# Performance work log

Hardware: AMD Instinct MI355X
Metric: run time of the kernel (lower is better)

## Reference

```python
import jax, jax.numpy as jnp
import numpy as np

H = 8        # n_heads (== n_kv_heads)
D = 128      # head_dim
WINDOW = 16  # sliding window (left); causal => right window = 0
EPS = 1e-6   # qk_norm_eps


def rms_norm(x, w, eps=EPS):
    # RMSNorm over last dim with learnable scale
    ms = jnp.mean(jnp.square(x), axis=-1, keepdims=True)
    return x * jax.lax.rsqrt(ms + eps) * w


def setup_inputs() -> dict:
    key = jax.random.key(0)
    ks = jax.random.split(key, 5)
    B, S, dim = 4, 2048, 1024
    scale = 1.0 / np.sqrt(dim)
    return {
        "x": jax.random.normal(ks[0], (B, S, dim), jnp.float32),
        "wq": jax.random.normal(ks[1], (dim, dim), jnp.float32) * scale,
        "wk": jax.random.normal(ks[2], (dim, dim), jnp.float32) * scale,
        "wv": jax.random.normal(ks[3], (dim, dim), jnp.float32) * scale,
        "wo": jax.random.normal(ks[4], (dim, dim), jnp.float32) * scale,
        "q_norm_w": jnp.ones((dim,), jnp.float32),
        "k_norm_w": jnp.ones((dim,), jnp.float32),
    }


def reference(x, wq, wk, wv, wo, q_norm_w, k_norm_w):
    B, S, dim = x.shape
    # projections (torch Linear: x @ W.T)
    xq = rms_norm(x @ wq.T, q_norm_w)
    xk = rms_norm(x @ wk.T, k_norm_w)
    xv = x @ wv.T
    q = xq.reshape(B, S, H, D)
    k = xk.reshape(B, S, H, D)
    v = xv.reshape(B, S, H, D)

    # ALiBi slopes for 8 heads (power of two): 2^-1 .. 2^-8
    slopes = jnp.exp2(-jnp.arange(1, H + 1, dtype=jnp.float32))
    pos = jnp.arange(S)
    rel = pos[None, :] - pos[:, None]          # [S, S], rel[i, j] = j - i
    bias = slopes[:, None, None] * rel.astype(x.dtype)   # [H, S, S]
    masked = (rel > 0) | (rel < -WINDOW)       # causal + sliding window
    bias = jnp.where(masked[None], -jnp.inf, bias)

    scores = jnp.einsum('bqhd,bkhd->bhqk', q, k) / np.sqrt(D) + bias[None]
    attn = jax.nn.softmax(scores, axis=-1)
    out = jnp.einsum('bhqk,bkhd->bqhd', attn, v).reshape(B, S, H * D)
    return out @ wo.T
```

## Files before the change

### kernel.cpp

```cpp
#include <hip/hip_runtime.h>
#include <math.h>

#define NHEADS 8
#define HDIM   128
#define WIN    16
#define DIM    1024
#define QKVDIM 3072
#define SEQ    2048
#define BATCH  4
#define MROWS  (BATCH * SEQ)
#define RMS_EPS 1e-6f

typedef __bf16 bf16x8 __attribute__((ext_vector_type(8)));
typedef unsigned short u16x8 __attribute__((ext_vector_type(8)));
typedef float  f32x4  __attribute__((ext_vector_type(4)));

__device__ __forceinline__ unsigned short f2b(float f) {
    union { float f; unsigned u; } c; c.f = f;
    return (unsigned short)((c.u + 0x7FFFu + ((c.u >> 16) & 1u)) >> 16);
}
__device__ __forceinline__ float b2f(unsigned short u) {
    union { unsigned u; float f; } c; c.u = ((unsigned)u) << 16; return c.f;
}

__device__ __forceinline__ void storec(unsigned short* p, float v) { *p = f2b(v); }
__device__ __forceinline__ void storec(float* p, float v) { *p = v; }

__global__ __launch_bounds__(256) void cast_all(const float* __restrict__ x,
                                                const float* __restrict__ w0,
                                                const float* __restrict__ w1,
                                                const float* __restrict__ w2,
                                                const float* __restrict__ w3,
                                                unsigned short* __restrict__ xb,
                                                unsigned short* __restrict__ wb)
{
    const int b = blockIdx.x;
    const int t = threadIdx.x;
    const float* src;
    unsigned short* dst;
    int i;
    if (b < 8192) {
        i = b * 256 + t;
        src = x; dst = xb;
    } else {
        const int bb = b - 8192;
        const int which = bb >> 10;
        i = (bb & 1023) * 256 + t;
        src = which == 0 ? w0 : which == 1 ? w1 : which == 2 ? w2 : w3;
        dst = wb + (size_t)which * DIM * DIM;
    }
    const float4 v = ((const float4*)src)[i];
    ushort4 o;
    o.x = f2b(v.x); o.y = f2b(v.y); o.z = f2b(v.z); o.w = f2b(v.w);
    ((ushort4*)dst)[i] = o;
}

template <typename TC>
__global__ __launch_bounds__(256) void gemm_nt_mfma(const unsigned short* __restrict__ A,
                                                    const unsigned short* __restrict__ B,
                                                    TC* __restrict__ C,
                                                    int M, int N, int K)
{
    __shared__ __align__(16) __bf16 As[128 * 32];
    __shared__ __align__(16) __bf16 Bs[128 * 32];

    const int t    = threadIdx.x;
    const int w    = t >> 6;
    const int lane = t & 63;
    const int wm   = w >> 1;
    const int wn   = w & 1;
    const int bm0  = blockIdx.y * 128;
    const int bn0  = blockIdx.x * 128;

    const int sr = lane >> 2;
    const int kc = (lane & 3) * 8;

    const unsigned short* gA0 = A + (size_t)(bm0 + w * 16 + sr) * K + kc;
    const unsigned short* gA1 = gA0 + (size_t)64 * K;
    const unsigned short* gB0 = B + (size_t)(bn0 + w * 16 + sr) * K + kc;
    const unsigned short* gB1 = gB0 + (size_t)64 * K;

    __bf16* lA0 = &As[(w * 16) * 32];
    __bf16* lA1 = &As[(w * 16 + 64) * 32];
    __bf16* lB0 = &Bs[(w * 16) * 32];
    __bf16* lB1 = &Bs[(w * 16 + 64) * 32];

    const int frow = lane & 15;
    const int fk   = (lane >> 4) * 8;

    f32x4 acc[4][4];
    #pragma unroll
    for (int i = 0; i < 4; ++i)
        #pragma unroll
        for (int j = 0; j < 4; ++j)
            #pragma unroll
            for (int e = 0; e < 4; ++e) acc[i][j][e] = 0.f;

    for (int kt = 0; kt < K; kt += 32) {
        __syncthreads();
        __builtin_amdgcn_global_load_lds((const __attribute__((address_space(1))) void*)(gA0 + kt),
                                         (__attribute__((address_space(3))) void*)lA0, 16, 0, 0);
        __builtin_amdgcn_global_load_lds((const __attribute__((address_space(1))) void*)(gA1 + kt),
                                         (__attribute__((address_space(3))) void*)lA1, 16, 0, 0);
        __builtin_amdgcn_global_load_lds((const __attribute__((address_space(1))) void*)(gB0 + kt),
                                         (__attribute__((address_space(3))) void*)lB0, 16, 0, 0);
        __builtin_amdgcn_global_load_lds((const __attribute__((address_space(1))) void*)(gB1 + kt),
                                         (__attribute__((address_space(3))) void*)lB1, 16, 0, 0);
        __syncthreads();

        bf16x8 af[4], bg[4];
        #pragma unroll
        for (int i = 0; i < 4; ++i) {
            af[i] = *(const bf16x8*)&As[(wm * 64 + i * 16 + frow) * 32 + fk];
            bg[i] = *(const bf16x8*)&Bs[(wn * 64 + i * 16 + frow) * 32 + fk];
        }
        #pragma unroll
        for (int i = 0; i < 4; ++i)
            #pragma unroll
            for (int j = 0; j < 4; ++j)
                acc[i][j] = __builtin_amdgcn_mfma_f32_16x16x32_bf16(af[i], bg[j], acc[i][j], 0, 0, 0);
    }

    const int m_base = bm0 + wm * 64;
    const int n_base = bn0 + wn * 64;
    const int col    = lane & 15;
    const int rquad  = (lane >> 4) * 4;
    #pragma unroll
    for (int i = 0; i < 4; ++i)
        #pragma unroll
        for (int r = 0; r < 4; ++r) {
            TC* crow = C + (size_t)(m_base + i * 16 + rquad + r) * N + n_base + col;
            #pragma unroll
            for (int j = 0; j < 4; ++j)
                storec(crow + j * 16, acc[i][j][r]);
        }
}

__global__ __launch_bounds__(256) void rmsnorm2(unsigned short* __restrict__ xqkv,
                                                const float* __restrict__ qw,
                                                const float* __restrict__ kw)
{
    const int row   = blockIdx.x;
    const int which = blockIdx.y;
    const int t     = threadIdx.x;
    unsigned short* xr = xqkv + (size_t)row * QKVDIM + which * DIM;
    const float* w = which ? kw : qw;

    const ushort4 u = ((const ushort4*)xr)[t];
    const float4 v = make_float4(b2f(u.x), b2f(u.y), b2f(u.z), b2f(u.w));
    float ss = v.x * v.x + v.y * v.y + v.z * v.z + v.w * v.w;
    #pragma unroll
    for (int off = 32; off > 0; off >>= 1) ss += __shfl_xor(ss, off, 64);

    __shared__ float red[4];
    if ((t & 63) == 0) red[t >> 6] = ss;
    __syncthreads();
    const float total = red[0] + red[1] + red[2] + red[3];
    const float scale = rsqrtf(total * (1.0f / DIM) + RMS_EPS);

    const float4 wv = ((const float4*)w)[t];
    ushort4 o;
    o.x = f2b(v.x * scale * wv.x);
    o.y = f2b(v.y * scale * wv.y);
    o.z = f2b(v.z * scale * wv.z);
    o.w = f2b(v.w * scale * wv.w);
    ((ushort4*)xr)[t] = o;
}

__global__ __launch_bounds__(256) void attn_mfma(const unsigned short* __restrict__ qkv,
                                                 unsigned short* __restrict__ o)
{
    __shared__ __align__(16) unsigned short Klds[80 * 136];
    __shared__ __align__(16) unsigned short Vt[128 * 88];
    __shared__ __align__(16) unsigned short Plds[4 * 16 * 40];

    const int t  = threadIdx.x;
    const int qb = blockIdx.x;
    const int h  = blockIdx.y;
    const int r0 = qb * 64;
    const int i0 = r0 & (SEQ - 1);
    const int bb = r0 - i0;

    const unsigned short* kg = qkv + DIM + h * HDIM;
    const unsigned short* vg = qkv + 2 * DIM + h * HDIM;

    #pragma unroll
    for (int it = 0; it < 5; ++it) {
        const int c = it * 256 + t;
        {
            const int lr = c >> 4, c8 = c & 15;
            const int ks = i0 - 16 + lr;
            const int rc = ks < 0 ? 0 : ks;
            const u16x8 kv = *(const u16x8*)(kg + (size_t)(bb + rc) * QKVDIM + c8 * 8);
            *(u16x8*)&Klds[lr * 136 + c8 * 8] = kv;
        }
        {
            const int c8 = c / 80, lr = c - c8 * 80;
            const int ks = i0 - 16 + lr;
            const int rc = ks < 0 ? 0 : ks;
            const u16x8 vv = *(const u16x8*)(vg + (size_t)(bb + rc) * QKVDIM + c8 * 8);
            #pragma unroll
            for (int e = 0; e < 8; ++e)
                Vt[(c8 * 8 + e) * 88 + lr] = vv[e];
        }
    }
    __syncthreads();

    const int w    = t >> 6;
    const int lane = t & 63;
    const int frow = lane & 15;
    const int quad = lane >> 4;
    const int fk   = quad * 8;

    f32x4 s0 = {0.f, 0.f, 0.f, 0.f}, s1 = {0.f, 0.f, 0.f, 0.f};
    const unsigned short* qg = qkv + h * HDIM;
    const size_t qrow = (size_t)(r0 + w * 16 + frow) * QKVDIM;
    #pragma unroll
    for (int kt = 0; kt < 4; ++kt) {
        const bf16x8 af = *(const bf16x8*)(qg + qrow + kt * 32 + fk);
        const bf16x8 b0 = *(const bf16x8*)&Klds[(w * 16 + frow) * 136 + kt * 32 + fk];
        const bf16x8 b1 = *(const bf16x8*)&Klds[(w * 16 + 16 + frow) * 136 + kt * 32 + fk];
        s0 = __builtin_amdgcn_mfma_f32_16x16x32_bf16(af, b0, s0, 0, 0, 0);
        s1 = __builtin_amdgcn_mfma_f32_16x16x32_bf16(af, b1, s1, 0, 0, 0);
    }

    const float scl   = 0.088388347648318447f;
    const float slope = exp2f(-(float)(h + 1));
    const bool  lead  = (i0 == 0) && (w == 0);
    const int   col   = frow;
    float inv[4];
    #pragma unroll
    for (int r = 0; r < 4; ++r) {
        const int m = quad * 4 + r;
        float v0 = (col < m || lead) ? -1e30f : s0[r] * scl + slope * (float)(col - 16 - m);
        float v1 = (col > m)         ? -1e30f : s1[r] * scl + slope * (float)(col - m);
        float mx = fmaxf(v0, v1);
        #pragma unroll
        for (int off = 1; off < 16; off <<= 1) mx = fmaxf(mx, __shfl_xor(mx, off, 64));
        const float e0 = __expf(v0 - mx);
        const float e1 = __expf(v1 - mx);
        float sm = e0 + e1;
        #pragma unroll
        for (int off = 1; off < 16; off <<= 1) sm += __shfl_xor(sm, off, 64);
        inv[r] = 1.0f / sm;
        Plds[(w * 16 + m) * 40 + col]      = f2b(e0);
        Plds[(w * 16 + m) * 40 + 16 + col] = f2b(e1);
    }

    const bf16x8 pf = *(const bf16x8*)&Plds[(w * 16 + frow) * 40 + fk];
    f32x4 oa[8];
    #pragma unroll
    for (int nt = 0; nt < 8; ++nt) {
        oa[nt][0] = 0.f; oa[nt][1] = 0.f; oa[nt][2] = 0.f; oa[nt][3] = 0.f;
        const bf16x8 vf = *(const bf16x8*)&Vt[(nt * 16 + frow) * 88 + w * 16 + fk];
        oa[nt] = __builtin_amdgcn_mfma_f32_16x16x32_bf16(pf, vf, oa[nt], 0, 0, 0);
    }

    #pragma unroll
    for (int nt = 0; nt < 8; ++nt)
        #pragma unroll
        for (int r = 0; r < 4; ++r) {
            const int m = quad * 4 + r;
            o[(size_t)(r0 + w * 16 + m) * DIM + h * HDIM + nt * 16 + col] =
                f2b(oa[nt][r] * inv[r]);
        }
}

extern "C" void kernel_launch(void* const* d_in, const int* in_sizes, int n_in,
                              void* d_out, int out_size, void* d_ws, size_t ws_size,
                              hipStream_t stream)
{
    const float* x  = (const float*)d_in[0];
    const float* wq = (const float*)d_in[1];
    const float* wk = (const float*)d_in[2];
    const float* wv = (const float*)d_in[3];
    const float* wo = (const float*)d_in[4];
    const float* qw = (const float*)d_in[5];
    const float* kw = (const float*)d_in[6];
    float* out = (float*)d_out;

    unsigned short* xb   = (unsigned short*)d_ws;
    unsigned short* wb   = xb + (size_t)MROWS * DIM;
    unsigned short* xqkv = wb + (size_t)4 * DIM * DIM;
    unsigned short* ob   = xqkv + (size_t)MROWS * QKVDIM;
    unsigned short* wob  = wb + (size_t)3 * DIM * DIM;

    cast_all<<<12288, 256, 0, stream>>>(x, wq, wk, wv, wo, xb, wb);

    gemm_nt_mfma<unsigned short><<<dim3(QKVDIM / 128, MROWS / 128), 256, 0, stream>>>(
        xb, wb, xqkv, MROWS, QKVDIM, DIM);

    rmsnorm2<<<dim3(MROWS, 2), 256, 0, stream>>>(xqkv, qw, kw);

    attn_mfma<<<dim3(MROWS / 64, NHEADS), 256, 0, stream>>>(xqkv, ob);

    gemm_nt_mfma<float><<<dim3(DIM / 128, MROWS / 128), 256, 0, stream>>>(
        ob, wob, out, MROWS, DIM, DIM);
}
```

Baseline: 229.4 us.

## Fuse RMSNorm into GEMM epilogue and attention load; widen GEMM K tile with swizzle

The separate rmsnorm kernel is removed. The QKV GEMM epilogue now accumulates per-row sums of squares into a workspace buffer with atomics, and the attention kernel applies the normalization scale and weights to Q and K as it loads them. The cast kernel zeroes that buffer. Separately, the GEMM K tile doubles from 32 to 64, with an XOR-swizzled LDS layout to avoid bank conflicts and half as many barriers. This removes a full read-modify-write pass over Q and K, at the cost of atomics and extra math in attention. The sums of squares come from fp32 accumulators rather than rounded bf16, and K rows are renormalized redundantly across query blocks.

```diff
diff --git a/kernel.cpp b/kernel.cpp
--- a/kernel.cpp
+++ b/kernel.cpp
@@ -22,6 +22,9 @@
 __device__ __forceinline__ float b2f(unsigned short u) {
     union { unsigned u; float f; } c; c.u = ((unsigned)u) << 16; return c.f;
 }
+__device__ __forceinline__ bf16x8 u2b(u16x8 u) {
+    union { u16x8 u; bf16x8 b; } c; c.u = u; return c.b;
+}
 
 __device__ __forceinline__ void storec(unsigned short* p, float v) { *p = f2b(v); }
 __device__ __forceinline__ void storec(float* p, float v) { *p = v; }
@@ -32,10 +35,15 @@
                                                 const float* __restrict__ w2,
                                                 const float* __restrict__ w3,
                                                 unsigned short* __restrict__ xb,
-                                                unsigned short* __restrict__ wb)
+                                                unsigned short* __restrict__ wb,
+                                                float* __restrict__ sumsq)
 {
     const int b = blockIdx.x;
     const int t = threadIdx.x;
+    if (b >= 12288) {
+        ((float4*)sumsq)[(b - 12288) * 256 + t] = make_float4(0.f, 0.f, 0.f, 0.f);
+        return;
+    }
     const float* src;
     unsigned short* dst;
     int i;
@@ -59,10 +67,11 @@
 __global__ __launch_bounds__(256) void gemm_nt_mfma(const unsigned short* __restrict__ A,
                                                     const unsigned short* __restrict__ B,
                                                     TC* __restrict__ C,
+                                                    float* __restrict__ sumsq,
                                                     int M, int N, int K)
 {
-    __shared__ __align__(16) __bf16 As[128 * 32];
-    __shared__ __align__(16) __bf16 Bs[128 * 32];
+    __shared__ __align__(16) __bf16 As[128 * 64];
+    __shared__ __align__(16) __bf16 Bs[128 * 64];
 
     const int t    = threadIdx.x;
     const int w    = t >> 6;
@@ -72,21 +81,17 @@
     const int bm0  = blockIdx.y * 128;
     const int bn0  = blockIdx.x * 128;
 
-    const int sr = lane >> 2;
-    const int kc = (lane & 3) * 8;
-
-    const unsigned short* gA0 = A + (size_t)(bm0 + w * 16 + sr) * K + kc;
-    const unsigned short* gA1 = gA0 + (size_t)64 * K;
-    const unsigned short* gB0 = B + (size_t)(bn0 + w * 16 + sr) * K + kc;
-    const unsigned short* gB1 = gB0 + (size_t)64 * K;
-
-    __bf16* lA0 = &As[(w * 16) * 32];
-    __bf16* lA1 = &As[(w * 16 + 64) * 32];
-    __bf16* lB0 = &Bs[(w * 16) * 32];
-    __bf16* lB1 = &Bs[(w * 16 + 64) * 32];
+    const int lrow   = lane >> 3;
+    const int lchunk = (lane & 7) ^ (lrow & 7);
+    const size_t laneoff = (size_t)lrow * K + lchunk * 8;
+
+    const unsigned short* gA = A + (size_t)bm0 * K + laneoff;
+    const unsigned short* gB = B + (size_t)bn0 * K + laneoff;
 
     const int frow = lane & 15;
-    const int fk   = (lane >> 4) * 8;
+    const int quad = lane >> 4;
+    const int cs0 = ((quad    ) ^ (frow & 7)) * 8;
+    const int cs1 = ((quad + 4) ^ (frow & 7)) * 8;
 
     f32x4 acc[4][4];
     #pragma unroll
@@ -96,35 +101,41 @@
             #pragma unroll
             for (int e = 0; e < 4; ++e) acc[i][j][e] = 0.f;
 
-    for (int kt = 0; kt < K; kt += 32) {
+    for (int kt = 0; kt < K; kt += 64) {
         __syncthreads();
-        __builtin_amdgcn_global_load_lds((const __attribute__((address_space(1))) void*)(gA0 + kt),
-                                         (__attribute__((address_space(3))) void*)lA0, 16, 0, 0);
-        __builtin_amdgcn_global_load_lds((const __attribute__((address_space(1))) void*)(gA1 + kt),
-                                         (__attribute__((address_space(3))) void*)lA1, 16, 0, 0);
-        __builtin_amdgcn_global_load_lds((const __attribute__((address_space(1))) void*)(gB0 + kt),
-                                         (__attribute__((address_space(3))) void*)lB0, 16, 0, 0);
-        __builtin_amdgcn_global_load_lds((const __attribute__((address_space(1))) void*)(gB1 + kt),
-                                         (__attribute__((address_space(3))) void*)lB1, 16, 0, 0);
+        #pragma unroll
+        for (int s = 0; s < 4; ++s) {
+            const int seg = w * 4 + s;
+            __builtin_amdgcn_global_load_lds(
+                (const __attribute__((address_space(1))) void*)(gA + (size_t)seg * 8 * K + kt),
+                (__attribute__((address_space(3))) void*)&As[seg * 512], 16, 0, 0);
+            __builtin_amdgcn_global_load_lds(
+                (const __attribute__((address_space(1))) void*)(gB + (size_t)seg * 8 * K + kt),
+                (__attribute__((address_space(3))) void*)&Bs[seg * 512], 16, 0, 0);
+        }
         __syncthreads();
 
-        bf16x8 af[4], bg[4];
-        #pragma unroll
-        for (int i = 0; i < 4; ++i) {
-            af[i] = *(const bf16x8*)&As[(wm * 64 + i * 16 + frow) * 32 + fk];
-            bg[i] = *(const bf16x8*)&Bs[(wn * 64 + i * 16 + frow) * 32 + fk];
-        }
-        #pragma unroll
-        for (int i = 0; i < 4; ++i)
-            #pragma unroll
-            for (int j = 0; j < 4; ++j)
-                acc[i][j] = __builtin_amdgcn_mfma_f32_16x16x32_bf16(af[i], bg[j], acc[i][j], 0, 0, 0);
+        #pragma unroll
+        for (int sub = 0; sub < 2; ++sub) {
+            const int cs = sub ? cs1 : cs0;
+            bf16x8 af[4], bg[4];
+            #pragma unroll
+            for (int i = 0; i < 4; ++i) {
+                af[i] = *(const bf16x8*)&As[(wm * 64 + i * 16 + frow) * 64 + cs];
+                bg[i] = *(const bf16x8*)&Bs[(wn * 64 + i * 16 + frow) * 64 + cs];
+            }
+            #pragma unroll
+            for (int i = 0; i < 4; ++i)
+                #pragma unroll
+                for (int j = 0; j < 4; ++j)
+                    acc[i][j] = __builtin_amdgcn_mfma_f32_16x16x32_bf16(af[i], bg[j], acc[i][j], 0, 0, 0);
+        }
     }
 
     const int m_base = bm0 + wm * 64;
     const int n_base = bn0 + wn * 64;
-    const int col    = lane & 15;
-    const int rquad  = (lane >> 4) * 4;
+    const int col    = frow;
+    const int rquad  = quad * 4;
     #pragma unroll
     for (int i = 0; i < 4; ++i)
         #pragma unroll
@@ -134,40 +145,29 @@
             for (int j = 0; j < 4; ++j)
                 storec(crow + j * 16, acc[i][j][r]);
         }
-}
-
-__global__ __launch_bounds__(256) void rmsnorm2(unsigned short* __restrict__ xqkv,
-                                                const float* __restrict__ qw,
-                                                const float* __restrict__ kw)
-{
-    const int row   = blockIdx.x;
-    const int which = blockIdx.y;
-    const int t     = threadIdx.x;
-    unsigned short* xr = xqkv + (size_t)row * QKVDIM + which * DIM;
-    const float* w = which ? kw : qw;
-
-    const ushort4 u = ((const ushort4*)xr)[t];
-    const float4 v = make_float4(b2f(u.x), b2f(u.y), b2f(u.z), b2f(u.w));
-    float ss = v.x * v.x + v.y * v.y + v.z * v.z + v.w * v.w;
-    #pragma unroll
-    for (int off = 32; off > 0; off >>= 1) ss += __shfl_xor(ss, off, 64);
-
-    __shared__ float red[4];
-    if ((t & 63) == 0) red[t >> 6] = ss;
-    __syncthreads();
-    const float total = red[0] + red[1] + red[2] + red[3];
-    const float scale = rsqrtf(total * (1.0f / DIM) + RMS_EPS);
-
-    const float4 wv = ((const float4*)w)[t];
-    ushort4 o;
-    o.x = f2b(v.x * scale * wv.x);
-    o.y = f2b(v.y * scale * wv.y);
-    o.z = f2b(v.z * scale * wv.z);
-    o.w = f2b(v.w * scale * wv.w);
-    ((ushort4*)xr)[t] = o;
+
+    if (sumsq != nullptr && bn0 < 2 * DIM) {
+        const int which = bn0 >> 10;
+        #pragma unroll
+        for (int i = 0; i < 4; ++i)
+            #pragma unroll
+            for (int r = 0; r < 4; ++r) {
+                float p = acc[i][0][r] * acc[i][0][r] + acc[i][1][r] * acc[i][1][r]
+                        + acc[i][2][r] * acc[i][2][r] + acc[i][3][r] * acc[i][3][r];
+                p += __shfl_xor(p, 1, 64);
+                p += __shfl_xor(p, 2, 64);
+                p += __shfl_xor(p, 4, 64);
+                p += __shfl_xor(p, 8, 64);
+                if (frow == 0)
+                    atomicAdd(&sumsq[(size_t)(m_base + i * 16 + rquad + r) * 2 + which], p);
+            }
+    }
 }
 
 __global__ __launch_bounds__(256) void attn_mfma(const unsigned short* __restrict__ qkv,
+                                                 const float* __restrict__ sumsq,
+                                                 const float* __restrict__ qw,
+                                                 const float* __restrict__ kw,
                                                  unsigned short* __restrict__ o)
 {
     __shared__ __align__(16) unsigned short Klds[80 * 136];
@@ -191,8 +191,13 @@
             const int lr = c >> 4, c8 = c & 15;
             const int ks = i0 - 16 + lr;
             const int rc = ks < 0 ? 0 : ks;
+            const float ksc = rsqrtf(sumsq[(size_t)(bb + rc) * 2 + 1] * (1.0f / DIM) + RMS_EPS);
             const u16x8 kv = *(const u16x8*)(kg + (size_t)(bb + rc) * QKVDIM + c8 * 8);
-            *(u16x8*)&Klds[lr * 136 + c8 * 8] = kv;
+            u16x8 ko;
+            #pragma unroll
+            for (int e = 0; e < 8; ++e)
+                ko[e] = f2b(b2f(kv[e]) * ksc * kw[h * HDIM + c8 * 8 + e]);
+            *(u16x8*)&Klds[lr * 136 + c8 * 8] = ko;
         }
         {
             const int c8 = c / 80, lr = c - c8 * 80;
@@ -215,9 +220,15 @@
     f32x4 s0 = {0.f, 0.f, 0.f, 0.f}, s1 = {0.f, 0.f, 0.f, 0.f};
     const unsigned short* qg = qkv + h * HDIM;
     const size_t qrow = (size_t)(r0 + w * 16 + frow) * QKVDIM;
+    const float qsc = rsqrtf(sumsq[(size_t)(r0 + w * 16 + frow) * 2] * (1.0f / DIM) + RMS_EPS);
     #pragma unroll
     for (int kt = 0; kt < 4; ++kt) {
-        const bf16x8 af = *(const bf16x8*)(qg + qrow + kt * 32 + fk);
+        const u16x8 qa = *(const u16x8*)(qg + qrow + kt * 32 + fk);
+        u16x8 qn;
+        #pragma unroll
+        for (int e = 0; e < 8; ++e)
+            qn[e] = f2b(b2f(qa[e]) * qsc * qw[h * HDIM + kt * 32 + fk + e]);
+        const bf16x8 af = u2b(qn);
         const bf16x8 b0 = *(const bf16x8*)&Klds[(w * 16 + frow) * 136 + kt * 32 + fk];
         const bf16x8 b1 = *(const bf16x8*)&Klds[(w * 16 + 16 + frow) * 136 + kt * 32 + fk];
         s0 = __builtin_amdgcn_mfma_f32_16x16x32_bf16(af, b0, s0, 0, 0, 0);
@@ -283,17 +294,16 @@
     unsigned short* wb   = xb + (size_t)MROWS * DIM;
     unsigned short* xqkv = wb + (size_t)4 * DIM * DIM;
     unsigned short* ob   = xqkv + (size_t)MROWS * QKVDIM;
+    float*          ssq  = (float*)(ob + (size_t)MROWS * DIM);
     unsigned short* wob  = wb + (size_t)3 * DIM * DIM;
 
-    cast_all<<<12288, 256, 0, stream>>>(x, wq, wk, wv, wo, xb, wb);
+    cast_all<<<12304, 256, 0, stream>>>(x, wq, wk, wv, wo, xb, wb, ssq);
 
     gemm_nt_mfma<unsigned short><<<dim3(QKVDIM / 128, MROWS / 128), 256, 0, stream>>>(
-        xb, wb, xqkv, MROWS, QKVDIM, DIM);
-
-    rmsnorm2<<<dim3(MROWS, 2), 256, 0, stream>>>(xqkv, qw, kw);
-
-    attn_mfma<<<dim3(MROWS / 64, NHEADS), 256, 0, stream>>>(xqkv, ob);
+        xb, wb, xqkv, ssq, MROWS, QKVDIM, DIM);
+
+    attn_mfma<<<dim3(MROWS / 64, NHEADS), 256, 0, stream>>>(xqkv, ssq, qw, kw, ob);
 
     gemm_nt_mfma<float><<<dim3(DIM / 128, MROWS / 128), 256, 0, stream>>>(
-        ob, wob, out, MROWS, DIM, DIM);
-}
+        ob, wob, out, nullptr, MROWS, DIM, DIM);
+}
```

New measurement: 218.4 us. 4.8% less time.
